# Optimization experiments

Measured on AMD Instinct MI355X. Metric: run time of the kernel, lower is better.

The kernel has to match this reference:

```python
import jax, jax.numpy as jnp
import numpy as np

B, S, D, H, L, E, F, K, V = 4, 1024, 768, 12, 2, 8, 3072, 2, 50257
HD = D // H
EPS = 1e-6
N_TIME, N_LOC, N_ROAD, N_WEATHER = 288, 1000, 10, 8


def rmsnorm(x, w):
    return x / jnp.sqrt(jnp.mean(x * x, axis=-1, keepdims=True) + EPS) * w


def rope_cache(seq_len, dim):
    inv_freq = 1.0 / (10000.0 ** (jnp.arange(0, dim, 2, dtype=jnp.float32) / dim))
    freqs = jnp.arange(seq_len, dtype=jnp.float32)[:, None] * inv_freq[None, :]
    emb = jnp.concatenate([freqs, freqs], axis=-1)  # [S, HD]
    return jnp.cos(emb), jnp.sin(emb)


def rotate_half(x):
    h = x.shape[-1] // 2
    return jnp.concatenate([-x[..., h:], x[..., :h]], axis=-1)


def attention(x, Wq, Wk, Wv, Wo, cos, sin):
    b, s, d = x.shape
    def heads(w):
        return (x @ w).reshape(b, s, H, HD).transpose(0, 2, 1, 3)  # [B,H,S,HD]
    q, k, v = heads(Wq), heads(Wk), heads(Wv)
    c, sn = cos[None, None], sin[None, None]
    q = q * c + rotate_half(q) * sn
    k = k * c + rotate_half(k) * sn
    scores = jnp.einsum('bhqd,bhkd->bhqk', q, k) / jnp.sqrt(jnp.float32(HD))
    mask = jnp.tril(jnp.ones((s, s), dtype=bool))
    scores = jnp.where(mask[None, None], scores, jnp.finfo(scores.dtype).min)
    probs = jax.nn.softmax(scores, axis=-1)
    out = jnp.einsum('bhqk,bhkd->bhqd', probs, v)
    return out.transpose(0, 2, 1, 3).reshape(b, s, d) @ Wo


def moe(x, router_w, Wg, Wu, Wd):
    # x: [T, D]; top-k routed SwiGLU experts, combine weights renormalized over top-k
    probs = jax.nn.softmax(x @ router_w, axis=-1)              # [T, E]
    w, idx = jax.lax.top_k(probs, K)                           # [T, K]
    w = w / jnp.sum(w, axis=-1, keepdims=True)
    onehot = jax.nn.one_hot(idx, E, dtype=x.dtype)             # [T, K, E]
    combine = jnp.sum(onehot * w[..., None], axis=1)           # [T, E]
    out = jnp.zeros_like(x)
    for e in range(E):  # small fixed expert count
        h = jax.nn.silu(x @ Wg[e]) * (x @ Wu[e])               # [T, F]
        out = out + combine[:, e, None] * (h @ Wd[e])
    usage = jnp.mean(jnp.sum(onehot, axis=1), axis=0)          # [E]
    aux = jnp.sum(usage * jnp.mean(probs, axis=0)) * E
    return out, aux


def setup_inputs() -> dict:
    key = jax.random.key(0)
    ks = jax.random.split(key, 40)
    p = lambda i, shape: 0.02 * jax.random.normal(ks[i], shape, dtype=jnp.float32)
    inp = {}
    inp['input_ids'] = jax.random.randint(ks[0], (B, S), 0, V)
    inp['time_slots'] = jax.random.randint(ks[1], (B, 1), 0, N_TIME)
    inp['day_of_week'] = jax.random.randint(ks[2], (B, 1), 0, 7)
    inp['month'] = jax.random.randint(ks[3], (B, 1), 0, 12)
    inp['is_holiday'] = jax.random.randint(ks[4], (B, 1), 0, 2)
    inp['location_ids'] = jax.random.randint(ks[5], (B, 1), 0, N_LOC)
    inp['road_types'] = jax.random.randint(ks[6], (B, 1), 0, N_ROAD)
    inp['weather_states'] = jax.random.randint(ks[7], (B, 1), 0, N_WEATHER)
    inp['word_emb'] = p(8, (V, D))
    inp['time_emb'] = p(9, (N_TIME, D // 4))
    inp['dow_emb'] = p(10, (7, D // 4))
    inp['month_emb'] = p(11, (12, D // 4))
    inp['hol_emb'] = p(12, (2, D // 4))
    inp['loc_emb'] = p(13, (N_LOC, D // 2))
    inp['road_emb'] = p(14, (N_ROAD, D // 4))
    inp['weather_emb'] = p(15, (N_WEATHER, D // 4))
    inp['proj_w'] = p(16, (3 * D, D))
    inp['proj_b'] = jnp.zeros((D,), dtype=jnp.float32)
    inp['emb_norm_w'] = jnp.ones((D,), dtype=jnp.float32)
    inp['norm1_w'] = jnp.ones((L, D), dtype=jnp.float32)
    inp['Wq'] = p(17, (L, D, D))
    inp['Wk'] = p(18, (L, D, D))
    inp['Wv'] = p(19, (L, D, D))
    inp['Wo'] = p(20, (L, D, D))
    inp['norm2_w'] = jnp.ones((L, D), dtype=jnp.float32)
    inp['router_w'] = p(21, (L, D, E))
    inp['Wg'] = p(22, (L, E, D, F))
    inp['Wu'] = p(23, (L, E, D, F))
    inp['Wd'] = p(24, (L, E, F, D))
    inp['final_norm_w'] = jnp.ones((D,), dtype=jnp.float32)
    return inp


def reference(input_ids, time_slots, day_of_week, month, is_holiday, location_ids,
              road_types, weather_states, word_emb, time_emb, dow_emb, month_emb,
              hol_emb, loc_emb, road_emb, weather_emb, proj_w, proj_b, emb_norm_w,
              norm1_w, Wq, Wk, Wv, Wo, norm2_w, router_w, Wg, Wu, Wd, final_norm_w):
    b, s = input_ids.shape
    we = word_emb[input_ids]                                                  # [B,S,D]
    te = jnp.concatenate([time_emb[time_slots], dow_emb[day_of_week],
                          month_emb[month], hol_emb[is_holiday]], axis=-1)    # [B,1,D]
    le = loc_emb[location_ids]                                                # [B,1,D/2]
    ce = jnp.concatenate([road_emb[road_types], weather_emb[weather_states]], axis=-1)
    te = jnp.broadcast_to(te, (b, s, D))
    le = jnp.broadcast_to(le, (b, s, D // 2))
    ce = jnp.broadcast_to(ce, (b, s, D // 2))
    x = jnp.concatenate([we, te, le, ce], axis=-1) @ proj_w + proj_b          # [B,S,D]
    x = rmsnorm(x, emb_norm_w)
    cos, sin = rope_cache(s, HD)
    aux_total = jnp.float32(0.0)
    for l in range(L):
        x = x + attention(rmsnorm(x, norm1_w[l]), Wq[l], Wk[l], Wv[l], Wo[l], cos, sin)
        m, aux = moe(rmsnorm(x, norm2_w[l]).reshape(b * s, D),
                     router_w[l], Wg[l], Wu[l], Wd[l])
        x = x + m.reshape(b, s, D)
        aux_total = aux_total + aux
    x = rmsnorm(x, final_norm_w)
    return x, aux_total
```

## Files before the change

### kernel.cpp

```cpp
#include <hip/hip_runtime.h>
#include <math.h>


#define TTOK 4096
#define FDIM 3072
#define MAXSLOT 9216

typedef __attribute__((ext_vector_type(8))) short short8;
typedef __attribute__((ext_vector_type(4))) float f32x4;

__device__ __forceinline__ float bf2f(unsigned short u) {
  return __uint_as_float(((unsigned int)u) << 16);
}
__device__ __forceinline__ unsigned short f2bf(float f) {
  unsigned int u = __float_as_uint(f);
  u += 0x7fffu + ((u >> 16) & 1u);
  return (unsigned short)(u >> 16);
}
__device__ __forceinline__ void split3f(float a, unsigned short& h, unsigned short& m,
                                        unsigned short& l) {
  h = f2bf(a);
  float r = a - bf2f(h);
  m = f2bf(r);
  r -= bf2f(m);
// ... 149 lines not shown
  if ((tid & 63) == 0) wss[tid >> 6] = ss;
  __syncthreads();
  float tot = wss[0] + wss[1] + wss[2] + wss[3];
  float inv = 1.0f / sqrtf(tot / 768.0f + 1e-6f);
  float o0 = v0 * inv * w[tid], o1 = v1 * inv * w[tid + 256], o2 = v2 * inv * w[tid + 512];
  if (OUT != 1) {
    float* yr = yf + (size_t)t * 768;
    yr[tid] = o0; yr[tid + 256] = o1; yr[tid + 512] = o2;
  }
  if (OUT == 1 || OUT == 2) {
    unsigned short* yr = yb + (size_t)t * 768;
    unsigned short h, m;
    split2f(o0, h, m); yr[tid] = h;       yr[tid + pPS] = m;
    split2f(o1, h, m); yr[tid + 256] = h; yr[tid + 256 + pPS] = m;
    split2f(o2, h, m); yr[tid + 512] = h; yr[tid + 512 + pPS] = m;
  }
  if (OUT == 3) {
    unsigned short* yr = yb + (size_t)t * 768;
    yr[tid] = f2bf(o0); yr[tid + 256] = f2bf(o1); yr[tid + 512] = f2bf(o2);
  }
}

__global__ __launch_bounds__(256) void rope_apply_k(float* __restrict__ qkv,
                                                    const float* __restrict__ cosb,
                                                    const float* __restrict__ sinb) {
  int idx = blockIdx.x * 256 + threadIdx.x;
  int j = idx & 31;
  int hh = (idx >> 5) % 12;
  int t = idx / 384;
  int s = t & 1023;
  float c = cosb[s * 32 + j], sn = sinb[s * 32 + j];
  size_t base = (size_t)t * 2304 + hh * 64 + j;
  float q1 = qkv[base], q2 = qkv[base + 32];
  qkv[base]      = q1 * c - q2 * sn;
  qkv[base + 32] = q2 * c + q1 * sn;
  size_t kb = base + 768;
  float k1 = qkv[kb], k2 = qkv[kb + 32];
  qkv[kb]      = k1 * c - k2 * sn;
  qkv[kb + 32] = k2 * c + k1 * sn;
}

template <int EPI>
__global__ __launch_bounds__(256) void gemm3(const unsigned short* __restrict__ A, size_t aPS,
                                             const unsigned short* __restrict__ BT, size_t bPS,
                                             float* __restrict__ Cf, int N, int K,
                                             const float* __restrict__ rowBias) {
  __shared__ __align__(16) unsigned short As[3][4096];
  __shared__ __align__(16) unsigned short Bs[3][4096];
  int tid = threadIdx.x, w = tid >> 6, l = tid & 63, lr = l & 15, lg = l >> 4;
  int m0 = blockIdx.y * 128, n0 = blockIdx.x * 128;
  size_t aoff = (size_t)(m0 + 32 * w + lr) * K + lg * 8;
  size_t boff = (size_t)(n0 + 32 * w + lr) * K + lg * 8;
  size_t aoff1 = aoff + (size_t)16 * K, boff1 = boff + (size_t)16 * K;
  f32x4 acc[4][4];
  #pragma unroll
  for (int i = 0; i < 4; ++i)
    #pragma unroll
    for (int j = 0; j < 4; ++j) acc[i][j] = (f32x4){0.f, 0.f, 0.f, 0.f};
  int wr = w >> 1, wc = w & 1;
  for (int k0 = 0; k0 < K; k0 += 32) {
    #pragma unroll
    for (int p = 0; p < 3; ++p) {
      gload16(A + p * aPS + aoff + k0,  &As[p][1024 * w]);
      gload16(A + p * aPS + aoff1 + k0, &As[p][1024 * w + 512]);
      gload16(BT + p * bPS + boff + k0,  &Bs[p][1024 * w]);
      gload16(BT + p * bPS + boff1 + k0, &Bs[p][1024 * w + 512]);
    }
    __syncthreads();
    short8 af[3][4], bf[3][4];
    #pragma unroll
    for (int p = 0; p < 3; ++p)
      #pragma unroll
      for (int i = 0; i < 4; ++i) {
        af[p][i] = *(const short8*)(&As[p][(wr * 4 + i) * 512 + l * 8]);
        bf[p][i] = *(const short8*)(&Bs[p][(wc * 4 + i) * 512 + l * 8]);
      }
    MFMA_SPLIT3(acc)
    __syncthreads();
  }
  int colb = n0 + wc * 64 + lr;
  int rowb = m0 + wr * 64 + lg * 4;
  #pragma unroll
  for (int i = 0; i < 4; ++i)
    #pragma unroll
    for (int j = 0; j < 4; ++j) {
      int col = colb + j * 16;
      #pragma unroll
      for (int r = 0; r < 4; ++r) {
        int row = rowb + i * 16 + r;
        size_t idx = (size_t)row * N + col;
        float v = acc[i][j][r];
        if (EPI == 0)      Cf[idx] = v;
        else if (EPI == 2) Cf[idx] += v;
        else               Cf[idx] = v + rowBias[(row >> 10) * 768 + col];
      }
    }
}

template <int EPI>
__global__ __launch_bounds__(256) void gemm2(const unsigned short* __restrict__ A, size_t aPS,
                                             const unsigned short* __restrict__ BT, size_t bPS,
                                             float* __restrict__ Cf, int N, int K) {
  __shared__ __align__(16) unsigned short As[2][4096];
  __shared__ __align__(16) unsigned short Bs[2][4096];
  int tid = threadIdx.x, w = tid >> 6, l = tid & 63, lr = l & 15, lg = l >> 4;
  int m0 = blockIdx.y * 128, n0 = blockIdx.x * 128;
  size_t aoff = (size_t)(m0 + 32 * w + lr) * K + lg * 8;
  size_t boff = (size_t)(n0 + 32 * w + lr) * K + lg * 8;
  size_t aoff1 = aoff + (size_t)16 * K, boff1 = boff + (size_t)16 * K;
  f32x4 acc[4][4];
  #pragma unroll
  for (int i = 0; i < 4; ++i)
    #pragma unroll
    for (int j = 0; j < 4; ++j) acc[i][j] = (f32x4){0.f, 0.f, 0.f, 0.f};
  int wr = w >> 1, wc = w & 1;
  for (int k0 = 0; k0 < K; k0 += 32) {
    #pragma unroll
    for (int p = 0; p < 2; ++p) {
      gload16(A + p * aPS + aoff + k0,  &As[p][1024 * w]);
      gload16(A + p * aPS + aoff1 + k0, &As[p][1024 * w + 512]);
      gload16(BT + p * bPS + boff + k0,  &Bs[p][1024 * w]);
      gload16(BT + p * bPS + boff1 + k0, &Bs[p][1024 * w + 512]);
    }
    __syncthreads();
    short8 af[2][4], bf[2][4];
    #pragma unroll
    for (int p = 0; p < 2; ++p)
      #pragma unroll
      for (int i = 0; i < 4; ++i) {
        af[p][i] = *(const short8*)(&As[p][(wr * 4 + i) * 512 + l * 8]);
        bf[p][i] = *(const short8*)(&Bs[p][(wc * 4 + i) * 512 + l * 8]);
      }
    MFMA_SPLIT2(acc)
    __syncthreads();
  }
  int colb = n0 + wc * 64 + lr;
  int rowb = m0 + wr * 64 + lg * 4;
  #pragma unroll
  for (int i = 0; i < 4; ++i)
    #pragma unroll
    for (int j = 0; j < 4; ++j) {
      int col = colb + j * 16;
      #pragma unroll
      for (int r = 0; r < 4; ++r) {
        int row = rowb + i * 16 + r;
        size_t idx = (size_t)row * N + col;
        float v = acc[i][j][r];
        if (EPI == 0) Cf[idx] = v;
        else          Cf[idx] += v;
      }
    }
}

template <int FUSE>
__global__ __launch_bounds__(256) void gemm2_gu(const unsigned short* __restrict__ X3, size_t xPS,
    const unsigned short* __restrict__ W2, size_t wPS, float* __restrict__ gout,
    unsigned short* __restrict__ hout, size_t hPS, const float* __restrict__ gin,
    const int* __restrict__ slot_token, const int* __restrict__ offs,
    const unsigned short* __restrict__ zp) {
  __shared__ __align__(16) unsigned short As[2][4096];
  __shared__ __align__(16) unsigned short Bs[2][4096];
  int sb = blockIdx.y * 128;
  int n0 = blockIdx.x * 128;
  if (sb >= offs[8]) return;
  int e = 0;
  #pragma unroll
  for (int i = 1; i < 8; ++i) if (sb >= offs[i]) e = i;
  int tid = threadIdx.x, w = tid >> 6, l = tid & 63, lr = l & 15, lg = l >> 4;
  const unsigned short* WE = W2 + (size_t)e * FDIM * 768;
  int t0 = slot_token[sb + 32 * w + lr];
  int t1 = slot_token[sb + 32 * w + 16 + lr];
  const unsigned short* a0[2];
  const unsigned short* a1[2];
  #pragma unroll
  for (int p = 0; p < 2; ++p) {
    a0[p] = (t0 < 0 ? zp : X3 + p * xPS + (size_t)t0 * 768) + lg * 8;
    a1[p] = (t1 < 0 ? zp : X3 + p * xPS + (size_t)t1 * 768) + lg * 8;
  }
  size_t boff = (size_t)(n0 + 32 * w + lr) * 768 + lg * 8;
  size_t boff1 = boff + (size_t)16 * 768;
  f32x4 acc[4][4];
  #pragma unroll
  for (int i = 0; i < 4; ++i)
    #pragma unroll
    for (int j = 0; j < 4; ++j) acc[i][j] = (f32x4){0.f, 0.f, 0.f, 0.f};
  int wr = w >> 1, wc = w & 1;
  for (int k0 = 0; k0 < 768; k0 += 32) {
    #pragma unroll
    for (int p = 0; p < 2; ++p) {
      gload16(a0[p] + k0, &As[p][1024 * w]);
      gload16(a1[p] + k0, &As[p][1024 * w + 512]);
      gload16(WE + p * wPS + boff + k0,  &Bs[p][1024 * w]);
      gload16(WE + p * wPS + boff1 + k0, &Bs[p][1024 * w + 512]);
    }
    __syncthreads();
    short8 af[2][4], bf[2][4];
    #pragma unroll
    for (int p = 0; p < 2; ++p)
      #pragma unroll
      for (int i = 0; i < 4; ++i) {
        af[p][i] = *(const short8*)(&As[p][(wr * 4 + i) * 512 + l * 8]);
        bf[p][i] = *(const short8*)(&Bs[p][(wc * 4 + i) * 512 + l * 8]);
      }
    MFMA_SPLIT2(acc)
    __syncthreads();
  }
  int colb = n0 + wc * 64 + lr;
  int rowb = sb + wr * 64 + lg * 4;
  #pragma unroll
  for (int i = 0; i < 4; ++i)
    #pragma unroll
    for (int j = 0; j < 4; ++j) {
      int col = colb + j * 16;
      #pragma unroll
      for (int r = 0; r < 4; ++r) {
        size_t idx = (size_t)(rowb + i * 16 + r) * FDIM + col;
        float v = acc[i][j][r];
        if (FUSE == 0) gout[idx] = v;
        else {
          float g = gin[idx];
          float h = g / (1.0f + expf(-g)) * v;
          unsigned short hh, hm;
          split2f(h, hh, hm);
          hout[idx] = hh; hout[idx + hPS] = hm;
        }
      }
    }
}

__global__ __launch_bounds__(256) void gemm2_dn(const unsigned short* __restrict__ hpl, size_t hPS,
    const unsigned short* __restrict__ W2, size_t wPS, float* __restrict__ ob,
    const int* __restrict__ offs) {
  __shared__ __align__(16) unsigned short As[2][4096];
  __shared__ __align__(16) unsigned short Bs[2][4096];
  int sb = blockIdx.y * 128;
  int n0 = blockIdx.x * 128;
  if (sb >= offs[8]) return;
  int e = 0;
  #pragma unroll
  for (int i = 1; i < 8; ++i) if (sb >= offs[i]) e = i;
  int tid = threadIdx.x, w = tid >> 6, l = tid & 63, lr = l & 15, lg = l >> 4;
  const unsigned short* WE = W2 + (size_t)e * 768 * FDIM;
  size_t aoff = (size_t)(sb + 32 * w + lr) * FDIM + lg * 8;
  size_t aoff1 = aoff + (size_t)16 * FDIM;
  size_t boff = (size_t)(n0 + 32 * w + lr) * FDIM + lg * 8;
  size_t boff1 = boff + (size_t)16 * FDIM;
  f32x4 acc[4][4];
  #pragma unroll
  for (int i = 0; i < 4; ++i)
    #pragma unroll
    for (int j = 0; j < 4; ++j) acc[i][j] = (f32x4){0.f, 0.f, 0.f, 0.f};
  int wr = w >> 1, wc = w & 1;
  for (int k0 = 0; k0 < FDIM; k0 += 32) {
    #pragma unroll
    for (int p = 0; p < 2; ++p) {
      gload16(hpl + p * hPS + aoff + k0,  &As[p][1024 * w]);
      gload16(hpl + p * hPS + aoff1 + k0, &As[p][1024 * w + 512]);
      gload16(WE + p * wPS + boff + k0,  &Bs[p][1024 * w]);
      gload16(WE + p * wPS + boff1 + k0, &Bs[p][1024 * w + 512]);
    }
    __syncthreads();
    short8 af[2][4], bf[2][4];
    #pragma unroll
    for (int p = 0; p < 2; ++p)
      #pragma unroll
      for (int i = 0; i < 4; ++i) {
        af[p][i] = *(const short8*)(&As[p][(wr * 4 + i) * 512 + l * 8]);
        bf[p][i] = *(const short8*)(&Bs[p][(wc * 4 + i) * 512 + l * 8]);
      }
    MFMA_SPLIT2(acc)
    __syncthreads();
  }
  int colb = n0 + wc * 64 + lr;
  int rowb = sb + wr * 64 + lg * 4;
  #pragma unroll
  for (int i = 0; i < 4; ++i)
    #pragma unroll
    for (int j = 0; j < 4; ++j) {
      int col = colb + j * 16;
      #pragma unroll
      for (int r = 0; r < 4; ++r)
        ob[(size_t)(rowb + i * 16 + r) * 768 + col] = acc[i][j][r];
    }
}

__global__ __launch_bounds__(256) void gemm_gu2(const unsigned short* __restrict__ xnb,
    const unsigned short* __restrict__ wgT, const unsigned short* __restrict__ wuT,
    unsigned short* __restrict__ gub, const int* __restrict__ slot_token,
    const int* __restrict__ offs, const unsigned short* __restrict__ zp) {
  __shared__ __align__(16) unsigned short As[4096], Bs[4096];
  int sb = blockIdx.y * 128;
  int n0 = blockIdx.x * 128;
  if (sb >= offs[8]) return;
  int e = 0;
  #pragma unroll
  for (int i = 1; i < 8; ++i) if (sb >= offs[i]) e = i;
  int tid = threadIdx.x, w = tid >> 6, l = tid & 63, lr = l & 15, lg = l >> 4;
  int nl = (n0 < FDIM) ? n0 : (n0 - FDIM);
  const unsigned short* WE = ((n0 < FDIM) ? wgT : wuT) + (size_t)e * FDIM * 768;
  unsigned short* OB = (n0 < FDIM) ? gub : (gub + (size_t)MAXSLOT * FDIM);
  int t0 = slot_token[sb + 32 * w + lr];
  int t1 = slot_token[sb + 32 * w + 16 + lr];
  const unsigned short* ga0 = (t0 < 0 ? zp : xnb + (size_t)t0 * 768) + lg * 8;
  const unsigned short* ga1 = (t1 < 0 ? zp : xnb + (size_t)t1 * 768) + lg * 8;
  const unsigned short* gb0 = WE + (size_t)(nl + 32 * w + lr) * 768 + lg * 8;
  const unsigned short* gb1 = gb0 + 16 * 768;
  f32x4 acc[4][4];
  #pragma unroll
  for (int i = 0; i < 4; ++i)
    #pragma unroll
    for (int j = 0; j < 4; ++j) acc[i][j] = (f32x4){0.f, 0.f, 0.f, 0.f};
  int wr = w >> 1, wc = w & 1;
  for (int k0 = 0; k0 < 768; k0 += 32) {
    gload16(ga0 + k0, As + 1024 * w);
    gload16(ga1 + k0, As + 1024 * w + 512);
    gload16(gb0 + k0, Bs + 1024 * w);
    gload16(gb1 + k0, Bs + 1024 * w + 512);
    __syncthreads();
    short8 af[4], bf[4];
    #pragma unroll
    for (int i = 0; i < 4; ++i) af[i] = *(const short8*)(As + (wr * 4 + i) * 512 + l * 8);
    #pragma unroll
    for (int j = 0; j < 4; ++j) bf[j] = *(const short8*)(Bs + (wc * 4 + j) * 512 + l * 8);
    #pragma unroll
    for (int i = 0; i < 4; ++i)
      #pragma unroll
      for (int j = 0; j < 4; ++j)
        acc[i][j] = __builtin_amdgcn_mfma_f32_16x16x32_bf16(af[i], bf[j], acc[i][j], 0, 0, 0);
    __syncthreads();
  }
  int colb = nl + wc * 64 + lr;
  int rowb = sb + wr * 64 + lg * 4;
  #pragma unroll
  for (int i = 0; i < 4; ++i)
    #pragma unroll
    for (int j = 0; j < 4; ++j) {
      int col = colb + j * 16;
      #pragma unroll
      for (int r = 0; r < 4; ++r)
        OB[(size_t)(rowb + i * 16 + r) * FDIM + col] = f2bf(acc[i][j][r]);
    }
}

__global__ void silu_mul_k(const unsigned short* __restrict__ gub,
                           unsigned short* __restrict__ hb) {
  size_t i = ((size_t)blockIdx.x * 256 + threadIdx.x) * 8;
  const unsigned short* u = gub + (size_t)MAXSLOT * FDIM;
  ushort4 g0 = *(const ushort4*)(gub + i);
  ushort4 g1 = *(const ushort4*)(gub + i + 4);
  ushort4 u0 = *(const ushort4*)(u + i);
  ushort4 u1 = *(const ushort4*)(u + i + 4);
  float gf[8] = {bf2f(g0.x), bf2f(g0.y), bf2f(g0.z), bf2f(g0.w),
                 bf2f(g1.x), bf2f(g1.y), bf2f(g1.z), bf2f(g1.w)};
  float uf[8] = {bf2f(u0.x), bf2f(u0.y), bf2f(u0.z), bf2f(u0.w),
                 bf2f(u1.x), bf2f(u1.y), bf2f(u1.z), bf2f(u1.w)};
  ushort4 h0, h1;
  h0.x = f2bf(gf[0] / (1.0f + expf(-gf[0])) * uf[0]);
  h0.y = f2bf(gf[1] / (1.0f + expf(-gf[1])) * uf[1]);
  h0.z = f2bf(gf[2] / (1.0f + expf(-gf[2])) * uf[2]);
  h0.w = f2bf(gf[3] / (1.0f + expf(-gf[3])) * uf[3]);
  h1.x = f2bf(gf[4] / (1.0f + expf(-gf[4])) * uf[4]);
  h1.y = f2bf(gf[5] / (1.0f + expf(-gf[5])) * uf[5]);
  h1.z = f2bf(gf[6] / (1.0f + expf(-gf[6])) * uf[6]);
  h1.w = f2bf(gf[7] / (1.0f + expf(-gf[7])) * uf[7]);
  *(ushort4*)(hb + i) = h0;
  *(ushort4*)(hb + i + 4) = h1;
}

__global__ __launch_bounds__(256) void gemm_d(const unsigned short* __restrict__ hb,
    const unsigned short* __restrict__ wdT, unsigned short* __restrict__ ob,
    const int* __restrict__ offs) {
  __shared__ __align__(16) unsigned short As[4096], Bs[4096];
  int sb = blockIdx.y * 128;
  int n0 = blockIdx.x * 128;
  if (sb >= offs[8]) return;
  int e = 0;
  #pragma unroll
  for (int i = 1; i < 8; ++i) if (sb >= offs[i]) e = i;
  int tid = threadIdx.x, w = tid >> 6, l = tid & 63, lr = l & 15, lg = l >> 4;
  const unsigned short* ga0 = hb + (size_t)(sb + 32 * w + lr) * FDIM + lg * 8;
  const unsigned short* ga1 = ga0 + (size_t)16 * FDIM;
  const unsigned short* WdE = wdT + (size_t)e * 768 * FDIM;
  const unsigned short* gb0 = WdE + (size_t)(n0 + 32 * w + lr) * FDIM + lg * 8;
  const unsigned short* gb1 = gb0 + (size_t)16 * FDIM;
  f32x4 acc[4][4];
  #pragma unroll
  for (int i = 0; i < 4; ++i)
    #pragma unroll
    for (int j = 0; j < 4; ++j) acc[i][j] = (f32x4){0.f, 0.f, 0.f, 0.f};
  int wr = w >> 1, wc = w & 1;
  for (int k0 = 0; k0 < FDIM; k0 += 32) {
    gload16(ga0 + k0, As + 1024 * w);
    gload16(ga1 + k0, As + 1024 * w + 512);
    gload16(gb0 + k0, Bs + 1024 * w);
    gload16(gb1 + k0, Bs + 1024 * w + 512);
    __syncthreads();
    short8 af[4], bf[4];
    #pragma unroll
    for (int i = 0; i < 4; ++i) af[i] = *(const short8*)(As + (wr * 4 + i) * 512 + l * 8);
    #pragma unroll
    for (int j = 0; j < 4; ++j) bf[j] = *(const short8*)(Bs + (wc * 4 + j) * 512 + l * 8);
    #pragma unroll
    for (int i = 0; i < 4; ++i)
      #pragma unroll
      for (int j = 0; j < 4; ++j)
        acc[i][j] = __builtin_amdgcn_mfma_f32_16x16x32_bf16(af[i], bf[j], acc[i][j], 0, 0, 0);
    __syncthreads();
  }
  int colb = n0 + wc * 64 + lr;
  int rowb = sb + wr * 64 + lg * 4;
  #pragma unroll
  for (int i = 0; i < 4; ++i)
    #pragma unroll
    for (int j = 0; j < 4; ++j) {
      int col = colb + j * 16;
      #pragma unroll
      for (int r = 0; r < 4; ++r)
        ob[(size_t)(rowb + i * 16 + r) * 768 + col] = f2bf(acc[i][j][r]);
    }
}

__global__ __launch_bounds__(256) void attn_k(const float* __restrict__ qkv,
                                              unsigned short* __restrict__ ax2, size_t pPS) {
  int pr = blockIdx.x, h = blockIdx.y, b = blockIdx.z;
  int tid = threadIdx.x;
  int ty4 = (tid >> 4) << 2, tx4 = (tid & 15) << 2;
  __shared__ float qs[64][68];
  __shared__ float kps[64][68];
  __shared__ float vs[64][68];
  int lr = tid >> 2;
  int lc = (tid & 3) << 4;
  for (int half = 0; half < 2; ++half) {
    int qt = half ? (15 - pr) : pr;
    int q0 = qt << 6;
    size_t qbase = ((size_t)(b * 1024 + q0 + lr)) * 2304 + h * 64 + lc;
    #pragma unroll
    for (int i = 0; i < 4; ++i) {
      float4 v = *(const float4*)(qkv + qbase + 4 * i);
      qs[lc + 4 * i + 0][lr] = v.x;
      qs[lc + 4 * i + 1][lr] = v.y;
      qs[lc + 4 * i + 2][lr] = v.z;
      qs[lc + 4 * i + 3][lr] = v.w;
    }
    float acc[4][4];
    float m[4], l[4];
    #pragma unroll
    for (int i = 0; i < 4; ++i) {
      m[i] = -3.0e38f; l[i] = 0.0f;
      #pragma unroll
      for (int j = 0; j < 4; ++j) acc[i][j] = 0.0f;
    }
    for (int kt = 0; kt <= qt; ++kt) {
      int k0 = kt << 6;
      __syncthreads();
      size_t kb = ((size_t)(b * 1024 + k0 + lr)) * 2304 + 768 + h * 64 + lc;
      #pragma unroll
      for (int i = 0; i < 4; ++i) {
        float4 kv = *(const float4*)(qkv + kb + 4 * i);
        kps[lc + 4 * i + 0][lr] = kv.x;
        kps[lc + 4 * i + 1][lr] = kv.y;
        kps[lc + 4 * i + 2][lr] = kv.z;
        kps[lc + 4 * i + 3][lr] = kv.w;
        *(float4*)&vs[lr][lc + 4 * i] = *(const float4*)(qkv + kb + 768 + 4 * i);
      }
      __syncthreads();
      float s[4][4];
      #pragma unroll
      for (int i = 0; i < 4; ++i)
        #pragma unroll
        for (int j = 0; j < 4; ++j) s[i][j] = 0.0f;
      #pragma unroll 8
      for (int d = 0; d < 64; ++d) {
        float4 qv = *(const float4*)&qs[d][ty4];
        float4 kv = *(const float4*)&kps[d][tx4];
        float qa[4] = {qv.x, qv.y, qv.z, qv.w};
        float ka[4] = {kv.x, kv.y, kv.z, kv.w};
        #pragma unroll
        for (int i = 0; i < 4; ++i)
          #pragma unroll
          for (int j = 0; j < 4; ++j) s[i][j] += qa[i] * ka[j];
      }
      bool diag = (kt == qt);
      #pragma unroll
      for (int i = 0; i < 4; ++i) {
        #pragma unroll
        for (int j = 0; j < 4; ++j) {
          if (diag && (tx4 + j > ty4 + i)) s[i][j] = -1.0e30f;
          else s[i][j] *= 0.125f;
        }
        float mx = fmaxf(fmaxf(s[i][0], s[i][1]), fmaxf(s[i][2], s[i][3]));
        mx = fmaxf(mx, __shfl_xor(mx, 1));
        mx = fmaxf(mx, __shfl_xor(mx, 2));
        mx = fmaxf(mx, __shfl_xor(mx, 4));
        mx = fmaxf(mx, __shfl_xor(mx, 8));
        float mnew = fmaxf(m[i], mx);
        float c = expf(m[i] - mnew);
        float rs = 0.0f;
        #pragma unroll
        for (int j = 0; j < 4; ++j) { s[i][j] = expf(s[i][j] - mnew); rs += s[i][j]; }
        rs += __shfl_xor(rs, 1);
        rs += __shfl_xor(rs, 2);
        rs += __shfl_xor(rs, 4);
        rs += __shfl_xor(rs, 8);
        l[i] = l[i] * c + rs;
        m[i] = mnew;
        #pragma unroll
        for (int j = 0; j < 4; ++j) acc[i][j] *= c;
      }
      __syncthreads();
      #pragma unroll
      for (int i = 0; i < 4; ++i)
        *(float4*)&kps[ty4 + i][tx4] = make_float4(s[i][0], s[i][1], s[i][2], s[i][3]);
      __syncthreads();
      #pragma unroll 4
      for (int kk = 0; kk < 16; ++kk) {
        float4 v0 = *(const float4*)&vs[(kk << 2) + 0][tx4];
        float4 v1 = *(const float4*)&vs[(kk << 2) + 1][tx4];
        float4 v2 = *(const float4*)&vs[(kk << 2) + 2][tx4];
        float4 v3 = *(const float4*)&vs[(kk << 2) + 3][tx4];
// ... 53 lines not shown
  if (lane == 0) {
    float mx = p[0];
    #pragma unroll
    for (int e = 1; e < 8; ++e) mx = fmaxf(mx, p[e]);
    float s = 0.0f;
    #pragma unroll
    for (int e = 0; e < 8; ++e) { p[e] = expf(p[e] - mx); s += p[e]; }
    float invs = 1.0f / s;
    #pragma unroll
    for (int e = 0; e < 8; ++e) p[e] *= invs;
    int i1 = 0; float v1 = p[0];
    #pragma unroll
    for (int e = 1; e < 8; ++e) if (p[e] > v1) { v1 = p[e]; i1 = e; }
    int i2 = (i1 == 0) ? 1 : 0; float v2 = p[i2];
    #pragma unroll
    for (int e = 0; e < 8; ++e) if (e != i1 && p[e] > v2) { v2 = p[e]; i2 = e; }
    float wsum = v1 + v2;
    tk_idx[t * 2] = i1; tk_idx[t * 2 + 1] = i2;
    tk_w[t * 2] = v1 / wsum; tk_w[t * 2 + 1] = v2 / wsum;
    atomicAdd(&bcnt[i1], 1); atomicAdd(&bcnt[i2], 1);
    #pragma unroll
    for (int e = 0; e < 8; ++e) atomicAdd(&bps[e], p[e]);
  }
  __syncthreads();
  if (tid < 8) {
    atomicAdd(&cnt[tid], bcnt[tid]);
    atomicAdd(&psum[tid], bps[tid]);
  }
}

__global__ void moe_offsets_k(const int* __restrict__ cnt, int* __restrict__ offs,
                              const float* __restrict__ psum, float* __restrict__ aux) {
  if (threadIdx.x == 0) {
    int o = 0; float a = 0.0f;
    for (int e = 0; e < 8; ++e) {
      offs[e] = o;
      o += (cnt[e] + 127) & ~127;
      a += ((float)cnt[e] / 4096.0f) * (psum[e] / 4096.0f);
    }
    offs[8] = o;
    aux[0] += a * 8.0f;
  }
}

__global__ void moe_fill_k(const int* __restrict__ tk_idx, const int* __restrict__ offs,
                           int* __restrict__ fill, int* __restrict__ slot_token,
                           int* __restrict__ tk_slot) {
  int i = blockIdx.x * 256 + threadIdx.x;
  int e = tk_idx[i];
  int pos = atomicAdd(&fill[e], 1);
  int slot = offs[e] + pos;
  slot_token[slot] = i >> 1;
  tk_slot[i] = slot;
}

template <int BF>
__global__ void moe_combine_k(float* __restrict__ x, const void* __restrict__ osv,
                              const int* __restrict__ tk_slot, const float* __restrict__ tk_w) {
  int t = blockIdx.x;
  int d = threadIdx.x << 2;
  int s0 = tk_slot[t * 2], s1 = tk_slot[t * 2 + 1];
  float w0 = tk_w[t * 2], w1 = tk_w[t * 2 + 1];
  float a0, a1, a2, a3, b0, b1, b2, b3;
  if (BF == 0) {
    const float* os = (const float*)osv;
    float4 a = *(const float4*)(os + (size_t)s0 * 768 + d);
    float4 b = *(const float4*)(os + (size_t)s1 * 768 + d);
    a0 = a.x; a1 = a.y; a2 = a.z; a3 = a.w;
    b0 = b.x; b1 = b.y; b2 = b.z; b3 = b.w;
  } else {
    const unsigned short* os = (const unsigned short*)osv;
    ushort4 a = *(const ushort4*)(os + (size_t)s0 * 768 + d);
    ushort4 b = *(const ushort4*)(os + (size_t)s1 * 768 + d);
    a0 = bf2f(a.x); a1 = bf2f(a.y); a2 = bf2f(a.z); a3 = bf2f(a.w);
    b0 = bf2f(b.x); b1 = bf2f(b.y); b2 = bf2f(b.z); b3 = bf2f(b.w);
  }
  float4 c = *(const float4*)(x + (size_t)t * 768 + d);
  c.x += w0 * a0 + w1 * b0;
  c.y += w0 * a1 + w1 * b1;
  c.z += w0 * a2 + w1 * b2;
  c.w += w0 * a3 + w1 * b3;
  *(float4*)(x + (size_t)t * 768 + d) = c;
}

__global__ void write_aux_k(const float* __restrict__ aux, float* __restrict__ out) {
  out[0] = aux[0];
}


extern "C" void kernel_launch(void* const* d_in, const int* in_sizes, int n_in,
                              void* d_out, int out_size, void* d_ws, size_t ws_size,
                              hipStream_t stream) {
  const int* input_ids      = (const int*)d_in[0];
  const int* time_slots     = (const int*)d_in[1];
  const int* day_of_week    = (const int*)d_in[2];
  const int* month          = (const int*)d_in[3];
  const int* is_holiday     = (const int*)d_in[4];
  const int* location_ids   = (const int*)d_in[5];
  const int* road_types     = (const int*)d_in[6];
  const int* weather_states = (const int*)d_in[7];
  const float* word_emb     = (const float*)d_in[8];
  const float* time_emb     = (const float*)d_in[9];
  const float* dow_emb      = (const float*)d_in[10];
  const float* month_emb    = (const float*)d_in[11];
  const float* hol_emb      = (const float*)d_in[12];
  const float* loc_emb      = (const float*)d_in[13];
  const float* road_emb     = (const float*)d_in[14];
  const float* weather_emb  = (const float*)d_in[15];
  const float* proj_w       = (const float*)d_in[16];
  const float* proj_b       = (const float*)d_in[17];
  const float* emb_norm_w   = (const float*)d_in[18];
  const float* norm1_w      = (const float*)d_in[19];
  const float* Wq           = (const float*)d_in[20];
  const float* Wk           = (const float*)d_in[21];
  const float* Wv           = (const float*)d_in[22];
  const float* Wo           = (const float*)d_in[23];
  const float* norm2_w      = (const float*)d_in[24];
  const float* router_w     = (const float*)d_in[25];
  const float* Wg           = (const float*)d_in[26];
  const float* Wu           = (const float*)d_in[27];
  const float* Wd           = (const float*)d_in[28];
  const float* final_norm_w = (const float*)d_in[29];
  float* out = (float*)d_out;

  const size_t TD = (size_t)TTOK * 768;
  const size_t REG = (size_t)MAXSLOT * FDIM * 4;
  const size_t HPS = (size_t)MAXSLOT * FDIM;
  char* base = (char*)d_ws;
  auto carve = [&](size_t bytes) { char* p = base; base += (bytes + 255) & ~(size_t)255; return p; };
  float* x    = (float*)carve(TD * 4);
  float* xn   = (float*)carve(TD * 4);
  float* cosb = (float*)carve(32768 * 4);
  float* sinb = (float*)carve(32768 * 4);
  float* ctx  = (float*)carve(4 * 1536 * 4);
  float* biasB= (float*)carve(4 * 768 * 4);
  float* tkw  = (float*)carve(8192 * 4);
  float* psum = (float*)carve(64);
  float* auxa = (float*)carve(64);
  int* cnt    = (int*)carve(64);
  int* fill   = (int*)carve(64);
  int* offs   = (int*)carve(64);
  int* tk_idx = (int*)carve(8192 * 4);
  int* tk_slot= (int*)carve(8192 * 4);
  int* slot_token = (int*)carve(MAXSLOT * 4);
  unsigned short* zp = (unsigned short*)carve(4096);
  unsigned short* xnb3 = (unsigned short*)carve(3 * TD * 2);
  char* QAH = carve(REG);
  char* GT  = carve(REG);
  char* Wr  = carve(REG);
  float* qkv = (float*)QAH;
  unsigned short* ax2 = (unsigned short*)(QAH + (size_t)TTOK * 2304 * 4);
  unsigned short* hpl = (unsigned short*)QAH;
  unsigned short* hb16 = (unsigned short*)QAH;
  float* gtmp = (float*)GT;
  float* obf = (float*)GT;
  unsigned short* gu16 = (unsigned short*)GT;
  unsigned short* ob16 = (unsigned short*)GT;
  unsigned short* wpl = (unsigned short*)Wr;

  const size_t PS_D = (size_t)768 * 768;
  const size_t PS_QKV = (size_t)2304 * 768;
  const size_t PS_E = (size_t)8 * FDIM * 768;

  hipMemsetAsync(auxa, 0, 64, stream);
  hipMemsetAsync(zp, 0, 4096, stream);
  rope_cache_k<<<dim3(1024), dim3(32), 0, stream>>>(cosb, sinb);
  build_ctx_k<<<dim3(4, 6), dim3(256), 0, stream>>>(time_slots, day_of_week, month, is_holiday,
      location_ids, road_types, weather_states, time_emb, dow_emb, month_emb, hol_emb,
      loc_emb, road_emb, weather_emb, ctx);
  build_bias_k<<<dim3(4, 3), dim3(256), 0, stream>>>(ctx, proj_w, proj_b, biasB);
  tconv3_k<<<dim3(12, 12, 1), dim3(64, 4), 0, stream>>>(proj_w, wpl, PS_D, 768, 768, 0, 0);
  gconv3_k<<<dim3(TTOK), dim3(192), 0, stream>>>(word_emb, input_ids, xnb3, TD);
  gemm3<3><<<dim3(6, 32), dim3(256), 0, stream>>>(xnb3, TD, wpl, PS_D, xn, 768, 768, biasB);
  rmsnorm_k<0><<<dim3(TTOK), dim3(256), 0, stream>>>(xn, emb_norm_w, x, nullptr, 0);

  for (int l = 0; l < 2; ++l) {
    const float* rw = router_w + (size_t)l * 768 * 8;
    tconv2_k<<<dim3(12, 12, 1), dim3(64, 4), 0, stream>>>(Wq + (size_t)l * PS_D, wpl, PS_QKV, 768, 768, 0, 0);
    tconv2_k<<<dim3(12, 12, 1), dim3(64, 4), 0, stream>>>(Wk + (size_t)l * PS_D, wpl + PS_D, PS_QKV, 768, 768, 0, 0);
    tconv2_k<<<dim3(12, 12, 1), dim3(64, 4), 0, stream>>>(Wv + (size_t)l * PS_D, wpl + 2 * PS_D, PS_QKV, 768, 768, 0, 0);
    rmsnorm_k<1><<<dim3(TTOK), dim3(256), 0, stream>>>(x, norm1_w + l * 768, nullptr, xnb3, TD);
    gemm2<0><<<dim3(18, 32), dim3(256), 0, stream>>>(xnb3, TD, wpl, PS_QKV, qkv, 2304, 768);
    rope_apply_k<<<dim3(6144), dim3(256), 0, stream>>>(qkv, cosb, sinb);
    attn_k<<<dim3(8, 12, 4), dim3(256), 0, stream>>>(qkv, ax2, TD);
    tconv2_k<<<dim3(12, 12, 1), dim3(64, 4), 0, stream>>>(Wo + (size_t)l * PS_D, wpl, PS_D, 768, 768, 0, 0);
    gemm2<2><<<dim3(6, 32), dim3(256), 0, stream>>>(ax2, TD, wpl, PS_D, x, 768, 768);

    if (l == 0)
      rmsnorm_k<2><<<dim3(TTOK), dim3(256), 0, stream>>>(x, norm2_w, xn, xnb3, TD);
    else
      rmsnorm_k<3><<<dim3(TTOK), dim3(256), 0, stream>>>(x, norm2_w + 768, xn, xnb3, TD);
    hipMemsetAsync(cnt, 0, 64, stream);
    hipMemsetAsync(fill, 0, 64, stream);
    hipMemsetAsync(psum, 0, 64, stream);
    hipMemsetAsync(slot_token, 0xFF, MAXSLOT * 4, stream);
    router_k<<<dim3(1024), dim3(256), 0, stream>>>(xn, rw, tk_idx, tkw, cnt, psum);
    moe_offsets_k<<<dim3(1), dim3(64), 0, stream>>>(cnt, offs, psum, auxa);
    moe_fill_k<<<dim3(32), dim3(256), 0, stream>>>(tk_idx, offs, fill, slot_token, tk_slot);
    if (l == 0) {
      tconv2_k<<<dim3(48, 12, 8), dim3(64, 4), 0, stream>>>(Wg, wpl, PS_E,
          768, FDIM, (size_t)768 * FDIM, (size_t)FDIM * 768);
      gemm2_gu<0><<<dim3(24, 72), dim3(256), 0, stream>>>(xnb3, TD, wpl, PS_E,
          gtmp, nullptr, 0, nullptr, slot_token, offs, zp);
      tconv2_k<<<dim3(48, 12, 8), dim3(64, 4), 0, stream>>>(Wu, wpl, PS_E,
          768, FDIM, (size_t)768 * FDIM, (size_t)FDIM * 768);
      gemm2_gu<1><<<dim3(24, 72), dim3(256), 0, stream>>>(xnb3, TD, wpl, PS_E,
          nullptr, hpl, HPS, gtmp, slot_token, offs, zp);
      tconv2_k<<<dim3(12, 48, 8), dim3(64, 4), 0, stream>>>(Wd, wpl, PS_E,
          FDIM, 768, (size_t)FDIM * 768, (size_t)768 * FDIM);
      gemm2_dn<<<dim3(6, 72), dim3(256), 0, stream>>>(hpl, HPS, wpl, PS_E, obf, offs);
      moe_combine_k<0><<<dim3(TTOK), dim3(192), 0, stream>>>(x, obf, tk_slot, tkw);
    } else {
      const float* wg1 = Wg + (size_t)8 * 768 * FDIM;
      const float* wu1 = Wu + (size_t)8 * 768 * FDIM;
      const float* wd1 = Wd + (size_t)8 * FDIM * 768;
      tconv_k<<<dim3(48, 12, 8), dim3(64, 4), 0, stream>>>(wg1, wpl,
          768, FDIM, (size_t)768 * FDIM, (size_t)FDIM * 768);
      tconv_k<<<dim3(48, 12, 8), dim3(64, 4), 0, stream>>>(wu1, wpl + PS_E,
          768, FDIM, (size_t)768 * FDIM, (size_t)FDIM * 768);
      gemm_gu2<<<dim3(48, 72), dim3(256), 0, stream>>>(xnb3, wpl, wpl + PS_E,
          gu16, slot_token, offs, zp);
      silu_mul_k<<<dim3((int)((size_t)MAXSLOT * FDIM / 2048)), dim3(256), 0, stream>>>(gu16, hb16);
      tconv_k<<<dim3(12, 48, 8), dim3(64, 4), 0, stream>>>(wd1, wpl,
          FDIM, 768, (size_t)FDIM * 768, (size_t)768 * FDIM);
      gemm_d<<<dim3(6, 72), dim3(256), 0, stream>>>(hb16, wpl, ob16, offs);
      moe_combine_k<1><<<dim3(TTOK), dim3(192), 0, stream>>>(x, ob16, tk_slot, tkw);
    }
  }

  rmsnorm_k<0><<<dim3(TTOK), dim3(256), 0, stream>>>(x, final_norm_w, out, nullptr, 0);
  write_aux_k<<<dim3(1), dim3(1), 0, stream>>>(auxa, out + TD);
}
```

Baseline: 2.145 ms.

## Fuse gate and up projections with SiLU-mul epilogue in MoE expert GEMMs

Each MoE gate/up kernel now computes both the gate and up accumulators in one block, running two sequential K loops, and applies SiLU(g)*u in the epilogue. This removes the fp32 gate intermediate write and read in layer 0, and the bf16 gate/up buffer plus the separate silu_mul kernel in layer 1. The cost is doubled accumulator registers (32 f32x4 per thread), which lowers occupancy. Half as many blocks are launched for layer 1, and the layer-0 up weights now need a separate staging buffer aliased onto GT.

```diff
diff --git a/kernel.cpp b/kernel.cpp
--- a/kernel.cpp
+++ b/kernel.cpp
@@ -325,10 +325,9 @@
     }
 }
 
-template <int FUSE>
-__global__ __launch_bounds__(256) void gemm2_gu(const unsigned short* __restrict__ X3, size_t xPS,
-    const unsigned short* __restrict__ W2, size_t wPS, float* __restrict__ gout,
-    unsigned short* __restrict__ hout, size_t hPS, const float* __restrict__ gin,
+__global__ __launch_bounds__(256) void gemm2_guf(const unsigned short* __restrict__ X3, size_t xPS,
+    const unsigned short* __restrict__ Wg2, const unsigned short* __restrict__ Wu2, size_t wPS,
+    unsigned short* __restrict__ hout, size_t hPS,
     const int* __restrict__ slot_token, const int* __restrict__ offs,
     const unsigned short* __restrict__ zp) {
   __shared__ __align__(16) unsigned short As[2][4096];
@@ -340,7 +339,8 @@
   #pragma unroll
   for (int i = 1; i < 8; ++i) if (sb >= offs[i]) e = i;
   int tid = threadIdx.x, w = tid >> 6, l = tid & 63, lr = l & 15, lg = l >> 4;
-  const unsigned short* WE = W2 + (size_t)e * FDIM * 768;
+  const unsigned short* WgE = Wg2 + (size_t)e * FDIM * 768;
+  const unsigned short* WuE = Wu2 + (size_t)e * FDIM * 768;
   int t0 = slot_token[sb + 32 * w + lr];
   int t1 = slot_token[sb + 32 * w + 16 + lr];
   const unsigned short* a0[2];
@@ -352,19 +352,22 @@
   }
   size_t boff = (size_t)(n0 + 32 * w + lr) * 768 + lg * 8;
   size_t boff1 = boff + (size_t)16 * 768;
-  f32x4 acc[4][4];
-  #pragma unroll
-  for (int i = 0; i < 4; ++i)
-    #pragma unroll
-    for (int j = 0; j < 4; ++j) acc[i][j] = (f32x4){0.f, 0.f, 0.f, 0.f};
   int wr = w >> 1, wc = w & 1;
+  f32x4 accg[4][4], accu[4][4];
+  #pragma unroll
+  for (int i = 0; i < 4; ++i)
+    #pragma unroll
+    for (int j = 0; j < 4; ++j) {
+      accg[i][j] = (f32x4){0.f, 0.f, 0.f, 0.f};
+      accu[i][j] = (f32x4){0.f, 0.f, 0.f, 0.f};
+    }
   for (int k0 = 0; k0 < 768; k0 += 32) {
     #pragma unroll
     for (int p = 0; p < 2; ++p) {
       gload16(a0[p] + k0, &As[p][1024 * w]);
       gload16(a1[p] + k0, &As[p][1024 * w + 512]);
-      gload16(WE + p * wPS + boff + k0,  &Bs[p][1024 * w]);
-      gload16(WE + p * wPS + boff1 + k0, &Bs[p][1024 * w + 512]);
+      gload16(WgE + p * wPS + boff + k0,  &Bs[p][1024 * w]);
+      gload16(WgE + p * wPS + boff1 + k0, &Bs[p][1024 * w + 512]);
     }
     __syncthreads();
     short8 af[2][4], bf[2][4];
@@ -375,7 +378,27 @@
         af[p][i] = *(const short8*)(&As[p][(wr * 4 + i) * 512 + l * 8]);
         bf[p][i] = *(const short8*)(&Bs[p][(wc * 4 + i) * 512 + l * 8]);
       }
-    MFMA_SPLIT2(acc)
+    MFMA_SPLIT2(accg)
+    __syncthreads();
+  }
+  for (int k0 = 0; k0 < 768; k0 += 32) {
+    #pragma unroll
+    for (int p = 0; p < 2; ++p) {
+      gload16(a0[p] + k0, &As[p][1024 * w]);
+      gload16(a1[p] + k0, &As[p][1024 * w + 512]);
+      gload16(WuE + p * wPS + boff + k0,  &Bs[p][1024 * w]);
+      gload16(WuE + p * wPS + boff1 + k0, &Bs[p][1024 * w + 512]);
+    }
+    __syncthreads();
+    short8 af[2][4], bf[2][4];
+    #pragma unroll
+    for (int p = 0; p < 2; ++p)
+      #pragma unroll
+      for (int i = 0; i < 4; ++i) {
+        af[p][i] = *(const short8*)(&As[p][(wr * 4 + i) * 512 + l * 8]);
+        bf[p][i] = *(const short8*)(&Bs[p][(wc * 4 + i) * 512 + l * 8]);
+      }
+    MFMA_SPLIT2(accu)
     __syncthreads();
   }
   int colb = n0 + wc * 64 + lr;
@@ -388,15 +411,11 @@
       #pragma unroll
       for (int r = 0; r < 4; ++r) {
         size_t idx = (size_t)(rowb + i * 16 + r) * FDIM + col;
-        float v = acc[i][j][r];
-        if (FUSE == 0) gout[idx] = v;
-        else {
-          float g = gin[idx];
-          float h = g / (1.0f + expf(-g)) * v;
-          unsigned short hh, hm;
-          split2f(h, hh, hm);
-          hout[idx] = hh; hout[idx + hPS] = hm;
-        }
+        float g = accg[i][j][r];
+        float h = g / (1.0f + expf(-g)) * accu[i][j][r];
+        unsigned short hh, hm;
+        split2f(h, hh, hm);
+        hout[idx] = hh; hout[idx + hPS] = hm;
       }
     }
 }
@@ -457,9 +476,9 @@
     }
 }
 
-__global__ __launch_bounds__(256) void gemm_gu2(const unsigned short* __restrict__ xnb,
+__global__ __launch_bounds__(256) void gemm_gu2f(const unsigned short* __restrict__ xnb,
     const unsigned short* __restrict__ wgT, const unsigned short* __restrict__ wuT,
-    unsigned short* __restrict__ gub, const int* __restrict__ slot_token,
+    unsigned short* __restrict__ hb, const int* __restrict__ slot_token,
     const int* __restrict__ offs, const unsigned short* __restrict__ zp) {
   __shared__ __align__(16) unsigned short As[4096], Bs[4096];
   int sb = blockIdx.y * 128;
@@ -469,26 +488,28 @@
   #pragma unroll
   for (int i = 1; i < 8; ++i) if (sb >= offs[i]) e = i;
   int tid = threadIdx.x, w = tid >> 6, l = tid & 63, lr = l & 15, lg = l >> 4;
-  int nl = (n0 < FDIM) ? n0 : (n0 - FDIM);
-  const unsigned short* WE = ((n0 < FDIM) ? wgT : wuT) + (size_t)e * FDIM * 768;
-  unsigned short* OB = (n0 < FDIM) ? gub : (gub + (size_t)MAXSLOT * FDIM);
+  const unsigned short* WgE = wgT + (size_t)e * FDIM * 768;
+  const unsigned short* WuE = wuT + (size_t)e * FDIM * 768;
   int t0 = slot_token[sb + 32 * w + lr];
   int t1 = slot_token[sb + 32 * w + 16 + lr];
   const unsigned short* ga0 = (t0 < 0 ? zp : xnb + (size_t)t0 * 768) + lg * 8;
   const unsigned short* ga1 = (t1 < 0 ? zp : xnb + (size_t)t1 * 768) + lg * 8;
-  const unsigned short* gb0 = WE + (size_t)(nl + 32 * w + lr) * 768 + lg * 8;
-  const unsigned short* gb1 = gb0 + 16 * 768;
-  f32x4 acc[4][4];
-  #pragma unroll
-  for (int i = 0; i < 4; ++i)
-    #pragma unroll
-    for (int j = 0; j < 4; ++j) acc[i][j] = (f32x4){0.f, 0.f, 0.f, 0.f};
+  size_t boff = (size_t)(n0 + 32 * w + lr) * 768 + lg * 8;
+  size_t boff1 = boff + (size_t)16 * 768;
   int wr = w >> 1, wc = w & 1;
+  f32x4 accg[4][4], accu[4][4];
+  #pragma unroll
+  for (int i = 0; i < 4; ++i)
+    #pragma unroll
+    for (int j = 0; j < 4; ++j) {
+      accg[i][j] = (f32x4){0.f, 0.f, 0.f, 0.f};
+      accu[i][j] = (f32x4){0.f, 0.f, 0.f, 0.f};
+    }
   for (int k0 = 0; k0 < 768; k0 += 32) {
     gload16(ga0 + k0, As + 1024 * w);
     gload16(ga1 + k0, As + 1024 * w + 512);
-    gload16(gb0 + k0, Bs + 1024 * w);
-    gload16(gb1 + k0, Bs + 1024 * w + 512);
+    gload16(WgE + boff + k0,  Bs + 1024 * w);
+    gload16(WgE + boff1 + k0, Bs + 1024 * w + 512);
     __syncthreads();
     short8 af[4], bf[4];
     #pragma unroll
@@ -499,10 +520,28 @@
     for (int i = 0; i < 4; ++i)
       #pragma unroll
       for (int j = 0; j < 4; ++j)
-        acc[i][j] = __builtin_amdgcn_mfma_f32_16x16x32_bf16(af[i], bf[j], acc[i][j], 0, 0, 0);
-    __syncthreads();
-  }
-  int colb = nl + wc * 64 + lr;
+        accg[i][j] = __builtin_amdgcn_mfma_f32_16x16x32_bf16(af[i], bf[j], accg[i][j], 0, 0, 0);
+    __syncthreads();
+  }
+  for (int k0 = 0; k0 < 768; k0 += 32) {
+    gload16(ga0 + k0, As + 1024 * w);
+    gload16(ga1 + k0, As + 1024 * w + 512);
+    gload16(WuE + boff + k0,  Bs + 1024 * w);
+    gload16(WuE + boff1 + k0, Bs + 1024 * w + 512);
+    __syncthreads();
+    short8 af[4], bf[4];
+    #pragma unroll
+    for (int i = 0; i < 4; ++i) af[i] = *(const short8*)(As + (wr * 4 + i) * 512 + l * 8);
+    #pragma unroll
+    for (int j = 0; j < 4; ++j) bf[j] = *(const short8*)(Bs + (wc * 4 + j) * 512 + l * 8);
+    #pragma unroll
+    for (int i = 0; i < 4; ++i)
+      #pragma unroll
+      for (int j = 0; j < 4; ++j)
+        accu[i][j] = __builtin_amdgcn_mfma_f32_16x16x32_bf16(af[i], bf[j], accu[i][j], 0, 0, 0);
+    __syncthreads();
+  }
+  int colb = n0 + wc * 64 + lr;
   int rowb = sb + wr * 64 + lg * 4;
   #pragma unroll
   for (int i = 0; i < 4; ++i)
@@ -510,34 +549,12 @@
     for (int j = 0; j < 4; ++j) {
       int col = colb + j * 16;
       #pragma unroll
-      for (int r = 0; r < 4; ++r)
-        OB[(size_t)(rowb + i * 16 + r) * FDIM + col] = f2bf(acc[i][j][r]);
-    }
-}
-
-__global__ void silu_mul_k(const unsigned short* __restrict__ gub,
-                           unsigned short* __restrict__ hb) {
-  size_t i = ((size_t)blockIdx.x * 256 + threadIdx.x) * 8;
-  const unsigned short* u = gub + (size_t)MAXSLOT * FDIM;
-  ushort4 g0 = *(const ushort4*)(gub + i);
-  ushort4 g1 = *(const ushort4*)(gub + i + 4);
-  ushort4 u0 = *(const ushort4*)(u + i);
-  ushort4 u1 = *(const ushort4*)(u + i + 4);
-  float gf[8] = {bf2f(g0.x), bf2f(g0.y), bf2f(g0.z), bf2f(g0.w),
-                 bf2f(g1.x), bf2f(g1.y), bf2f(g1.z), bf2f(g1.w)};
-  float uf[8] = {bf2f(u0.x), bf2f(u0.y), bf2f(u0.z), bf2f(u0.w),
-                 bf2f(u1.x), bf2f(u1.y), bf2f(u1.z), bf2f(u1.w)};
-  ushort4 h0, h1;
-  h0.x = f2bf(gf[0] / (1.0f + expf(-gf[0])) * uf[0]);
-  h0.y = f2bf(gf[1] / (1.0f + expf(-gf[1])) * uf[1]);
-  h0.z = f2bf(gf[2] / (1.0f + expf(-gf[2])) * uf[2]);
-  h0.w = f2bf(gf[3] / (1.0f + expf(-gf[3])) * uf[3]);
-  h1.x = f2bf(gf[4] / (1.0f + expf(-gf[4])) * uf[4]);
-  h1.y = f2bf(gf[5] / (1.0f + expf(-gf[5])) * uf[5]);
-  h1.z = f2bf(gf[6] / (1.0f + expf(-gf[6])) * uf[6]);
-  h1.w = f2bf(gf[7] / (1.0f + expf(-gf[7])) * uf[7]);
-  *(ushort4*)(hb + i) = h0;
-  *(ushort4*)(hb + i + 4) = h1;
+      for (int r = 0; r < 4; ++r) {
+        float g = accg[i][j][r];
+        hb[(size_t)(rowb + i * 16 + r) * FDIM + col] =
+            f2bf(g / (1.0f + expf(-g)) * accu[i][j][r]);
+      }
+    }
 }
 
 __global__ __launch_bounds__(256) void gemm_d(const unsigned short* __restrict__ hb,
@@ -897,9 +914,8 @@
   unsigned short* ax2 = (unsigned short*)(QAH + (size_t)TTOK * 2304 * 4);
   unsigned short* hpl = (unsigned short*)QAH;
   unsigned short* hb16 = (unsigned short*)QAH;
-  float* gtmp = (float*)GT;
+  unsigned short* wupl = (unsigned short*)GT;
   float* obf = (float*)GT;
-  unsigned short* gu16 = (unsigned short*)GT;
   unsigned short* ob16 = (unsigned short*)GT;
   unsigned short* wpl = (unsigned short*)Wr;
 
@@ -945,12 +961,10 @@
     if (l == 0) {
       tconv2_k<<<dim3(48, 12, 8), dim3(64, 4), 0, stream>>>(Wg, wpl, PS_E,
           768, FDIM, (size_t)768 * FDIM, (size_t)FDIM * 768);
-      gemm2_gu<0><<<dim3(24, 72), dim3(256), 0, stream>>>(xnb3, TD, wpl, PS_E,
-          gtmp, nullptr, 0, nullptr, slot_token, offs, zp);
-      tconv2_k<<<dim3(48, 12, 8), dim3(64, 4), 0, stream>>>(Wu, wpl, PS_E,
+      tconv2_k<<<dim3(48, 12, 8), dim3(64, 4), 0, stream>>>(Wu, wupl, PS_E,
           768, FDIM, (size_t)768 * FDIM, (size_t)FDIM * 768);
-      gemm2_gu<1><<<dim3(24, 72), dim3(256), 0, stream>>>(xnb3, TD, wpl, PS_E,
-          nullptr, hpl, HPS, gtmp, slot_token, offs, zp);
+      gemm2_guf<<<dim3(24, 72), dim3(256), 0, stream>>>(xnb3, TD, wpl, wupl, PS_E,
+          hpl, HPS, slot_token, offs, zp);
       tconv2_k<<<dim3(12, 48, 8), dim3(64, 4), 0, stream>>>(Wd, wpl, PS_E,
           FDIM, 768, (size_t)FDIM * 768, (size_t)768 * FDIM);
       gemm2_dn<<<dim3(6, 72), dim3(256), 0, stream>>>(hpl, HPS, wpl, PS_E, obf, offs);
@@ -963,9 +977,8 @@
           768, FDIM, (size_t)768 * FDIM, (size_t)FDIM * 768);
       tconv_k<<<dim3(48, 12, 8), dim3(64, 4), 0, stream>>>(wu1, wpl + PS_E,
           768, FDIM, (size_t)768 * FDIM, (size_t)FDIM * 768);
-      gemm_gu2<<<dim3(48, 72), dim3(256), 0, stream>>>(xnb3, wpl, wpl + PS_E,
-          gu16, slot_token, offs, zp);
-      silu_mul_k<<<dim3((int)((size_t)MAXSLOT * FDIM / 2048)), dim3(256), 0, stream>>>(gu16, hb16);
+      gemm_gu2f<<<dim3(24, 72), dim3(256), 0, stream>>>(xnb3, wpl, wpl + PS_E,
+          hb16, slot_token, offs, zp);
       tconv_k<<<dim3(12, 48, 8), dim3(64, 4), 0, stream>>>(wd1, wpl,
           FDIM, 768, (size_t)FDIM * 768, (size_t)768 * FDIM);
       gemm_d<<<dim3(6, 72), dim3(256), 0, stream>>>(hb16, wpl, ob16, offs);
```

After: 2.357 ms. +9.9%, slower.
